# Kernel tuning notes

Measured on AMD Instinct MI355X. Metric: run time of the kernel, lower is better.

## Reference

```python
import jax, jax.numpy as jnp
from jax import lax
import numpy as np

B, S = 256, 512
VOCAB, EMB_D = 50000, 300
POS_MAX, POS_D = 512, 16
CNN_OUT, K, NCLASS = 50, 5, 10


def setup_inputs() -> dict:
    key = jax.random.key(0)
    ks = jax.random.split(key, 7)
    return {
        "tokens": jax.random.randint(ks[0], (B, S), 0, VOCAB),
        "embed_table": jax.random.normal(ks[1], (VOCAB, EMB_D), jnp.float32),
        "pos_table": jax.random.normal(ks[2], (POS_MAX, POS_D), jnp.float32),
        "conv_w": jax.random.normal(ks[3], (CNN_OUT, EMB_D + 2 * POS_D, K), jnp.float32) * 0.05,
        "conv_b": jax.random.normal(ks[4], (CNN_OUT,), jnp.float32) * 0.05,
        "fc_w": jax.random.normal(ks[5], (NCLASS, CNN_OUT), jnp.float32) * 0.1,
        "fc_b": jax.random.normal(ks[6], (NCLASS,), jnp.float32) * 0.1,
        "entity1": 1,
        "entity2": 2,
    }


def _nearest_entity_dist(tokens, entity, max_pos):
    # Distance from each token to the nearest occurrence of `entity`,
    # clipped to [0, max_pos-1]; sentences without the entity clip to max.
    Sl = tokens.shape[1]
    idx = jnp.arange(Sl)
    occ = tokens == entity  # [B, S]
    big = 2 * Sl
    # nearest occurrence index to the left (running max) and right (running min)
    left = lax.cummax(jnp.where(occ, idx, -big), axis=1)
    right = lax.cummin(jnp.where(occ, idx, big), axis=1, reverse=True)
    dist = jnp.minimum(idx - left, right - idx)
    return jnp.clip(dist, 0, max_pos - 1)


def reference(tokens, embed_table, pos_table, conv_w, conv_b, fc_w, fc_b,
              entity1, entity2):
    emb = embed_table[tokens]                      # [B, S, EMB_D] gather
    pad = jnp.all(emb == 0.0, axis=-1)             # [B, S] zero-row mask
    feats = [emb]
    for ent in (entity1, entity2):
        d = _nearest_entity_dist(tokens, ent, pos_table.shape[0])
        pe = pos_table[d]                          # [B, S, POS_D]
        pe = jnp.where(pad[..., None], 0.0, pe)    # zero masked positions
        feats.append(pe)
    x = jnp.concatenate(feats, axis=-1)            # [B, S, 332]
    x = jnp.transpose(x, (0, 2, 1))                # [B, C, S]
    pad_hw = conv_w.shape[-1] // 2
    y = lax.conv_general_dilated(
        x, conv_w, window_strides=(1,), padding=[(pad_hw, pad_hw)],
        dimension_numbers=("NCH", "OIH", "NCH"))
    y = jax.nn.relu(y + conv_b[None, :, None])     # [B, 50, S]
    y = jnp.max(y, axis=2)                         # full-length max pool -> [B, 50]
    out = y @ fc_w.T + fc_b                        # [B, NCLASS]
    return out
```

## Files before the change

kernel.cpp:

```cpp
#include <hip/hip_runtime.h>
#include <hip/hip_bf16.h>

typedef __attribute__((ext_vector_type(8))) short short8;
typedef __attribute__((ext_vector_type(4))) float floatx4;

#define BB 256
#define SS 512
#define VOCAB 50000
#define EMB_D 300
#define POS_MAX 512
#define POS_D 16
#define CNN_OUT 50
#define KW 5
#define NCLASS 10
#define C_IN 332
#define NKS 55
#define MROWS 64
#define FROWS 68
#define FSTR 392
#define E2STR 320
#define NWF (NKS * 4 * 64 * 8)

__device__ __forceinline__ unsigned pack2bf(float x, float y) {
    __hip_bfloat162 h = __float22bfloat162_rn(make_float2(x, y));
    return *reinterpret_cast<unsigned*>(&h);
}

__device__ __forceinline__ unsigned short f2bf(float x) {
    unsigned u = __float_as_uint(x);
    u += 0x7FFF + ((u >> 16) & 1);
    return (unsigned short)(u >> 16);
}

__global__ __launch_bounds__(256) void k_cvt(const float* __restrict__ E,
                                             unsigned short* __restrict__ E2) {
    int row = blockIdx.x * 4 + (threadIdx.x >> 6);
    if (row >= VOCAB) return;
    int lane = threadIdx.x & 63;
    const float4* src = (const float4*)(E + (size_t)row * EMB_D);
    unsigned short* dst = E2 + (size_t)row * E2STR;
    float4 a = src[lane];
    *(uint2*)&dst[lane * 4] = make_uint2(pack2bf(a.x, a.y), pack2bf(a.z, a.w));
    if (lane < 11) {
        float4 bq = src[64 + lane];
        *(uint2*)&dst[256 + lane * 4] = make_uint2(pack2bf(bq.x, bq.y), pack2bf(bq.z, bq.w));
    } else if (lane < 16) {
        *(uint2*)&dst[300 + (lane - 11) * 4] = make_uint2(0u, 0u);
    }
}

__global__ __launch_bounds__(256) void k_prep(const float* __restrict__ conv_w,
                                              unsigned short* __restrict__ Wf,
                                              float* __restrict__ ymax) {
    int idx = blockIdx.x * 256 + threadIdx.x;
    if (idx < NWF) {
        int j = idx & 7, l = (idx >> 3) & 63, nb = (idx >> 9) & 3, ks = idx >> 11;
        int k = ks / 11;
        int c = (ks % 11) * 32 + ((l >> 4) << 3) + j;
        int col = nb * 16 + (l & 15);
        float v = 0.f;
        if (c < C_IN && col < CNN_OUT)
            v = conv_w[col * (C_IN * KW) + c * KW + k];
        Wf[idx] = f2bf(v);
    } else if (idx < NWF + BB * CNN_OUT) {
        ymax[idx - NWF] = 0.f;
    }
}

__global__ __launch_bounds__(512) void k_dist(const int* __restrict__ tokens,
                                              const int* __restrict__ e1p,
                                              const int* __restrict__ e2p,
                                              int* __restrict__ d1,
                                              int* __restrict__ d2) {
    __shared__ int cnt1, cnt2;
    __shared__ int lst1[SS], lst2[SS];
    int b = blockIdx.x, s = threadIdx.x;
    if (s == 0) { cnt1 = 0; cnt2 = 0; }
    __syncthreads();
    int tok = tokens[b * SS + s];
    int e1 = *e1p, e2 = *e2p;
    if (tok == e1) lst1[atomicAdd(&cnt1, 1)] = s;
    if (tok == e2) lst2[atomicAdd(&cnt2, 1)] = s;
    __syncthreads();
    int dd1 = POS_MAX - 1;
    int n1 = cnt1;
    for (int i = 0; i < n1; ++i) dd1 = min(dd1, abs(s - lst1[i]));
    int dd2 = POS_MAX - 1;
    int n2 = cnt2;
    for (int i = 0; i < n2; ++i) dd2 = min(dd2, abs(s - lst2[i]));
    d1[b * SS + s] = dd1;
    d2[b * SS + s] = dd2;
}

__global__ __launch_bounds__(256, 3) void k_fused(const int* __restrict__ tokens,
                                                  const int* __restrict__ d1,
                                                  const int* __restrict__ d2,
                                                  const unsigned short* __restrict__ E2,
                                                  const float* __restrict__ pos,
                                                  const unsigned short* __restrict__ Wf,
                                                  const float* __restrict__ conv_b,
                                                  float* __restrict__ ymax) {
    __shared__ __align__(16) short F[FROWS * FSTR];
    int tid = threadIdx.x, lane = tid & 63, w = tid >> 6;
    int b = blockIdx.x >> 3, sb = blockIdx.x & 7;
    int s0 = sb * MROWS;

    int q = tid & 3;
    for (int rr = tid >> 2; rr < FROWS; rr += 64) {
        int sp = s0 - 2 + rr;
        bool valid = (sp >= 0 && sp < SS);
        int t = valid ? tokens[b * SS + sp] : 0;
        const uint4* src = (const uint4*)(E2 + (size_t)t * E2STR);

        int dd = 0;
        if (q < 2)
            dd = valid ? (q == 0 ? d1[b * SS + sp] : d2[b * SS + sp]) : 0;

        uint4 v[10];
        #pragma unroll
        for (int i = 0; i < 10; ++i) {
            int c4 = q + i * 4;
            v[i] = valid ? src[c4] : make_uint4(0u, 0u, 0u, 0u);
        }
        float4 pv[4];
        if (q < 2) {
            const float4* ps = (const float4*)(pos + dd * POS_D);
            #pragma unroll
            for (int i = 0; i < 4; ++i)
                pv[i] = valid ? ps[i] : make_float4(0.f, 0.f, 0.f, 0.f);
        }

        unsigned nzb = 0;
        #pragma unroll
        for (int i = 0; i < 10; ++i)
            nzb |= (v[i].x | v[i].y | v[i].z | v[i].w);
        bool nz = (nzb & 0x7FFF7FFFu) != 0u;
        #pragma unroll
        for (int i = 0; i < 10; ++i) {
            int c4 = q + i * 4;
            if (c4 <= 36) {
                *(uint4*)&F[rr * FSTR + c4 * 8] = v[i];
            } else if (c4 == 37) {
                *(uint2*)&F[rr * FSTR + 296] = make_uint2(v[i].x, v[i].y);
            }
        }

        unsigned long long bal = __ballot(nz);
        int g = lane >> 2;
        bool rowz = (((bal >> (g * 4)) & 0xFULL) == 0ULL);

        if (q < 2) {
            float msk = (valid && !rowz) ? 1.f : 0.f;
            int cbase = EMB_D + q * POS_D;
            #pragma unroll
            for (int i = 0; i < 4; ++i)
                *(uint2*)&F[rr * FSTR + cbase + i * 4] =
                    make_uint2(pack2bf(pv[i].x * msk, pv[i].y * msk),
                               pack2bf(pv[i].z * msk, pv[i].w * msk));
        } else {
            int cbase = C_IN + (q - 2) * 10;
            #pragma unroll
            for (int i = 0; i < 5; ++i)
                *(unsigned*)&F[rr * FSTR + cbase + i * 2] = 0u;
        }
    }
    __syncthreads();

    floatx4 acc[4][4];
    #pragma unroll
    for (int mm = 0; mm < 4; ++mm)
        #pragma unroll
        for (int nn = 0; nn < 4; ++nn) acc[mm][nn] = (floatx4)0.f;

    int arow = lane & 15, achunk = (lane >> 4) * 8;
    const short8* Bp = (const short8*)Wf;
    int lo = w * 14;
    int hi = min(lo + 14, NKS);

    short8 bA[4], bB[4];
    #pragma unroll
    for (int nb = 0; nb < 4; ++nb)
        bA[nb] = Bp[(lo * 4 + nb) * 64 + lane];
    if (lo + 1 < hi) {
        #pragma unroll
        for (int nb = 0; nb < 4; ++nb)
            bB[nb] = Bp[((lo + 1) * 4 + nb) * 64 + lane];
    }

    auto step = [&](int ks, short8 (&bf)[4], int pfks) {
        int k = ks / 11, kc = ks % 11;
        const short* abase = &F[(arow + k) * FSTR + kc * 32 + achunk];
        #pragma unroll
        for (int mm = 0; mm < 4; ++mm) {
            short8 afrag = *(const short8*)(abase + mm * 16 * FSTR);
            #pragma unroll
            for (int nn = 0; nn < 4; ++nn)
                acc[mm][nn] = __builtin_amdgcn_mfma_f32_16x16x32_bf16(afrag, bf[nn], acc[mm][nn], 0, 0, 0);
        }
        if (pfks < hi) {
            #pragma unroll
            for (int nb = 0; nb < 4; ++nb)
                bf[nb] = Bp[(pfks * 4 + nb) * 64 + lane];
        }
    };

    int ks = lo;
    for (; ks + 1 < hi; ks += 2) {
        step(ks, bA, ks + 2);
        step(ks + 1, bB, ks + 3);
    }
    if (ks < hi) step(ks, bA, NKS);

    __syncthreads();
    float* R = (float*)F;
    floatx4 red[4];
    #pragma unroll
    for (int round = 0; round < 2; ++round) {
        #pragma unroll
        for (int i = 0; i < 2; ++i)
            #pragma unroll
            for (int nn = 0; nn < 4; ++nn)
                *(floatx4*)&R[((w * 8 + i * 4 + nn) * 64 + lane) * 4] = acc[round * 2 + i][nn];
        __syncthreads();
        #pragma unroll
        for (int i = 0; i < 2; ++i) {
            floatx4 t0 = *(floatx4*)&R[((0 * 8 + i * 4 + w) * 64 + lane) * 4];
            floatx4 t1 = *(floatx4*)&R[((1 * 8 + i * 4 + w) * 64 + lane) * 4];
            floatx4 t2 = *(floatx4*)&R[((2 * 8 + i * 4 + w) * 64 + lane) * 4];
            floatx4 t3 = *(floatx4*)&R[((3 * 8 + i * 4 + w) * 64 + lane) * 4];
            red[round * 2 + i] = (t0 + t1) + (t2 + t3);
        }
        if (round == 0) __syncthreads();
    }

    int col = w * 16 + (lane & 15);
    float bias = (col < CNN_OUT) ? conv_b[col] : 0.f;
    float m = 0.f;
    #pragma unroll
    for (int mi = 0; mi < 4; ++mi)
        #pragma unroll
        for (int rg = 0; rg < 4; ++rg)
            m = fmaxf(m, red[mi][rg] + bias);
    m = fmaxf(m, __shfl_xor(m, 16));
    m = fmaxf(m, __shfl_xor(m, 32));
    if ((lane >> 4) == 0 && col < CNN_OUT)
        atomicMax((int*)ymax + b * CNN_OUT + col, __float_as_int(m));
}

__global__ __launch_bounds__(64) void k_fc(const float* __restrict__ ymax,
                                           const float* __restrict__ fc_w,
                                           const float* __restrict__ fc_b,
                                           float* __restrict__ out) {
    int b = blockIdx.x, n = threadIdx.x;
    if (n < NCLASS) {
        float a = fc_b[n];
        #pragma unroll
        for (int o = 0; o < CNN_OUT; ++o)
            a += ymax[b * CNN_OUT + o] * fc_w[n * CNN_OUT + o];
        out[b * NCLASS + n] = a;
    }
}

extern "C" void kernel_launch(void* const* d_in, const int* in_sizes, int n_in,
                              void* d_out, int out_size, void* d_ws, size_t ws_size,
                              hipStream_t stream) {
    const int*   tokens  = (const int*)  d_in[0];
    const float* embed   = (const float*)d_in[1];
    const float* pos     = (const float*)d_in[2];
    const float* conv_w  = (const float*)d_in[3];
    const float* conv_b  = (const float*)d_in[4];
    const float* fc_w    = (const float*)d_in[5];
    const float* fc_b    = (const float*)d_in[6];
    const int*   e1p     = (const int*)  d_in[7];
    const int*   e2p     = (const int*)  d_in[8];
    float* out = (float*)d_out;

    char* ws = (char*)d_ws;
    size_t off = 0;
    unsigned short* E2 = (unsigned short*)(ws + off); off += (size_t)VOCAB * E2STR * 2;
    unsigned short* Wf = (unsigned short*)(ws + off); off += (size_t)NWF * 2;
    int*   d1     = (int*)  (ws + off); off += (size_t)BB * SS * 4;
    int*   d2     = (int*)  (ws + off); off += (size_t)BB * SS * 4;
    float* ymax   = (float*)(ws + off); off += (size_t)BB * CNN_OUT * 4;
    (void)ws_size; (void)in_sizes; (void)n_in; (void)out_size;

    hipLaunchKernelGGL(k_cvt, dim3((VOCAB + 3) / 4), dim3(256), 0, stream, embed, E2);
    {
        int total = NWF + BB * CNN_OUT;
        hipLaunchKernelGGL(k_prep, dim3((total + 255) / 256), dim3(256), 0, stream,
                           conv_w, Wf, ymax);
    }
    hipLaunchKernelGGL(k_dist, dim3(BB), dim3(512), 0, stream, tokens, e1p, e2p, d1, d2);
    hipLaunchKernelGGL(k_fused, dim3(BB * (SS / MROWS)), dim3(256), 0, stream,
                       tokens, d1, d2, E2, pos, Wf, conv_b, ymax);
    hipLaunchKernelGGL(k_fc, dim3(BB), dim3(64), 0, stream, ymax, fc_w, fc_b, out);
}
```

Baseline: 67.33 us.

## Make fused conv kernel persistent over tiles with double-buffered LDS prefetch

The fused conv kernel now runs 512 blocks, each walking 8 tiles of 32 rows with two LDS buffers. The gathers for the next tile are issued into registers before the MFMA loop and written to shared memory afterwards, so global latency overlaps compute. The zero-row pad mask is precomputed per vocab row in the conversion kernel, so it no longer needs a per-row ballot. In exchange each tile has more block-wide barriers and B fragments are reloaded every tile. Occupancy drops to 2 blocks per CU, and 512 blocks may underfill the GPU.

```diff
diff --git a/kernel.cpp b/kernel.cpp
--- a/kernel.cpp
+++ b/kernel.cpp
@@ -15,10 +15,13 @@
 #define NCLASS 10
 #define C_IN 332
 #define NKS 55
-#define MROWS 64
-#define FROWS 68
+#define MROWS 32
+#define TILES 8
+#define FROWS 36
 #define FSTR 392
 #define E2STR 320
+#define NCH 38
+#define NEV (FROWS * NCH)
 #define NWF (NKS * 4 * 64 * 8)
 
 __device__ __forceinline__ unsigned pack2bf(float x, float y) {
@@ -33,20 +36,28 @@
 }
 
 __global__ __launch_bounds__(256) void k_cvt(const float* __restrict__ E,
-                                             unsigned short* __restrict__ E2) {
+                                             unsigned short* __restrict__ E2,
+                                             int* __restrict__ rowz) {
     int row = blockIdx.x * 4 + (threadIdx.x >> 6);
     if (row >= VOCAB) return;
     int lane = threadIdx.x & 63;
     const float4* src = (const float4*)(E + (size_t)row * EMB_D);
     unsigned short* dst = E2 + (size_t)row * E2STR;
     float4 a = src[lane];
+    unsigned nzb = __float_as_uint(a.x) | __float_as_uint(a.y) |
+                   __float_as_uint(a.z) | __float_as_uint(a.w);
     *(uint2*)&dst[lane * 4] = make_uint2(pack2bf(a.x, a.y), pack2bf(a.z, a.w));
     if (lane < 11) {
         float4 bq = src[64 + lane];
+        nzb |= __float_as_uint(bq.x) | __float_as_uint(bq.y) |
+               __float_as_uint(bq.z) | __float_as_uint(bq.w);
         *(uint2*)&dst[256 + lane * 4] = make_uint2(pack2bf(bq.x, bq.y), pack2bf(bq.z, bq.w));
     } else if (lane < 16) {
         *(uint2*)&dst[300 + (lane - 11) * 4] = make_uint2(0u, 0u);
     }
+    bool nz = (nzb & 0x7FFFFFFFu) != 0u;
+    unsigned long long bal = __ballot(nz);
+    if (lane == 0) rowz[row] = (bal == 0ULL) ? 1 : 0;
 }
 
 __global__ __launch_bounds__(256) void k_prep(const float* __restrict__ conv_w,
@@ -92,155 +103,180 @@
     d2[b * SS + s] = dd2;
 }
 
-__global__ __launch_bounds__(256, 3) void k_fused(const int* __restrict__ tokens,
+__global__ __launch_bounds__(256, 2) void k_fused(const int* __restrict__ tokens,
                                                   const int* __restrict__ d1,
                                                   const int* __restrict__ d2,
+                                                  const int* __restrict__ rowz,
                                                   const unsigned short* __restrict__ E2,
                                                   const float* __restrict__ pos,
                                                   const unsigned short* __restrict__ Wf,
                                                   const float* __restrict__ conv_b,
                                                   float* __restrict__ ymax) {
-    __shared__ __align__(16) short F[FROWS * FSTR];
+    __shared__ __align__(16) short Fbuf[2][FROWS * FSTR];
     int tid = threadIdx.x, lane = tid & 63, w = tid >> 6;
-    int b = blockIdx.x >> 3, sb = blockIdx.x & 7;
-    int s0 = sb * MROWS;
-
-    int q = tid & 3;
-    for (int rr = tid >> 2; rr < FROWS; rr += 64) {
-        int sp = s0 - 2 + rr;
-        bool valid = (sp >= 0 && sp < SS);
-        int t = valid ? tokens[b * SS + sp] : 0;
-        const uint4* src = (const uint4*)(E2 + (size_t)t * E2STR);
-
-        int dd = 0;
-        if (q < 2)
-            dd = valid ? (q == 0 ? d1[b * SS + sp] : d2[b * SS + sp]) : 0;
-
-        uint4 v[10];
-        #pragma unroll
-        for (int i = 0; i < 10; ++i) {
-            int c4 = q + i * 4;
-            v[i] = valid ? src[c4] : make_uint4(0u, 0u, 0u, 0u);
-        }
-        float4 pv[4];
-        if (q < 2) {
-            const float4* ps = (const float4*)(pos + dd * POS_D);
-            #pragma unroll
-            for (int i = 0; i < 4; ++i)
-                pv[i] = valid ? ps[i] : make_float4(0.f, 0.f, 0.f, 0.f);
-        }
-
-        unsigned nzb = 0;
-        #pragma unroll
-        for (int i = 0; i < 10; ++i)
-            nzb |= (v[i].x | v[i].y | v[i].z | v[i].w);
-        bool nz = (nzb & 0x7FFF7FFFu) != 0u;
-        #pragma unroll
-        for (int i = 0; i < 10; ++i) {
-            int c4 = q + i * 4;
-            if (c4 <= 36) {
-                *(uint4*)&F[rr * FSTR + c4 * 8] = v[i];
-            } else if (c4 == 37) {
-                *(uint2*)&F[rr * FSTR + 296] = make_uint2(v[i].x, v[i].y);
-            }
-        }
-
-        unsigned long long bal = __ballot(nz);
-        int g = lane >> 2;
-        bool rowz = (((bal >> (g * 4)) & 0xFULL) == 0ULL);
-
-        if (q < 2) {
-            float msk = (valid && !rowz) ? 1.f : 0.f;
-            int cbase = EMB_D + q * POS_D;
-            #pragma unroll
-            for (int i = 0; i < 4; ++i)
-                *(uint2*)&F[rr * FSTR + cbase + i * 4] =
-                    make_uint2(pack2bf(pv[i].x * msk, pv[i].y * msk),
-                               pack2bf(pv[i].z * msk, pv[i].w * msk));
-        } else {
-            int cbase = C_IN + (q - 2) * 10;
-            #pragma unroll
-            for (int i = 0; i < 5; ++i)
-                *(unsigned*)&F[rr * FSTR + cbase + i * 2] = 0u;
-        }
-    }
+    int b = blockIdx.x >> 1, half = blockIdx.x & 1;
+    int base = half * (MROWS * TILES);
+
+    const int* trow = tokens + b * SS;
+    const int* d1r = d1 + b * SS;
+    const int* d2r = d2 + b * SS;
+
+    short* cur = Fbuf[0];
+    short* nxt = Fbuf[1];
+
+    uint4 ev[6];
+    float4 pv[2];
+    float pmsk[2];
+
+    auto issue = [&](int srow) {
+        #pragma unroll
+        for (int j = 0; j < 6; ++j) {
+            int idx = tid + j * 256;
+            ev[j] = make_uint4(0u, 0u, 0u, 0u);
+            if (idx < NEV) {
+                int row = idx / NCH, ch = idx % NCH;
+                int sp = srow - 2 + row;
+                bool valid = (sp >= 0 && sp < SS);
+                if (valid) {
+                    int t = trow[sp];
+                    ev[j] = ((const uint4*)(E2 + (size_t)t * E2STR))[ch];
+                }
+            }
+        }
+        #pragma unroll
+        for (int j = 0; j < 2; ++j) {
+            int idx = tid + j * 256;
+            pv[j] = make_float4(0.f, 0.f, 0.f, 0.f);
+            pmsk[j] = 0.f;
+            if (idx < FROWS * 8) {
+                int row = idx >> 3, q = idx & 7;
+                int sp = srow - 2 + row;
+                bool valid = (sp >= 0 && sp < SS);
+                int table = q >> 2, i = q & 3;
+                if (valid) {
+                    int t = trow[sp];
+                    int rz = rowz[t];
+                    int dd = table ? d2r[sp] : d1r[sp];
+                    pmsk[j] = rz ? 0.f : 1.f;
+                    pv[j] = ((const float4*)(pos + dd * POS_D))[i];
+                }
+            }
+        }
+    };
+
+    auto commit = [&](short* Fb) {
+        #pragma unroll
+        for (int j = 0; j < 6; ++j) {
+            int idx = tid + j * 256;
+            if (idx < NEV) {
+                int row = idx / NCH, ch = idx % NCH;
+                if (ch <= 36)
+                    *(uint4*)&Fb[row * FSTR + ch * 8] = ev[j];
+                else
+                    *(uint2*)&Fb[row * FSTR + 296] = make_uint2(ev[j].x, ev[j].y);
+            }
+        }
+        #pragma unroll
+        for (int j = 0; j < 2; ++j) {
+            int idx = tid + j * 256;
+            if (idx < FROWS * 8) {
+                int row = idx >> 3, q = idx & 7;
+                int table = q >> 2, i = q & 3;
+                float mk = pmsk[j];
+                *(uint2*)&Fb[row * FSTR + EMB_D + table * POS_D + i * 4] =
+                    make_uint2(pack2bf(pv[j].x * mk, pv[j].y * mk),
+                               pack2bf(pv[j].z * mk, pv[j].w * mk));
+            }
+        }
+        #pragma unroll
+        for (int j = 0; j < 2; ++j) {
+            int idx = tid + j * 256;
+            if (idx < FROWS * 10) {
+                int row = idx / 10, dw = idx % 10;
+                *(unsigned*)&Fb[row * FSTR + C_IN + dw * 2] = 0u;
+            }
+        }
+    };
+
+    issue(base);
+    commit(cur);
     __syncthreads();
-
-    floatx4 acc[4][4];
-    #pragma unroll
-    for (int mm = 0; mm < 4; ++mm)
-        #pragma unroll
-        for (int nn = 0; nn < 4; ++nn) acc[mm][nn] = (floatx4)0.f;
 
     int arow = lane & 15, achunk = (lane >> 4) * 8;
     const short8* Bp = (const short8*)Wf;
     int lo = w * 14;
     int hi = min(lo + 14, NKS);
-
-    short8 bA[4], bB[4];
-    #pragma unroll
-    for (int nb = 0; nb < 4; ++nb)
-        bA[nb] = Bp[(lo * 4 + nb) * 64 + lane];
-    if (lo + 1 < hi) {
+    float m = -1e30f;
+
+    for (int ti = 0; ti < TILES; ++ti) {
+        if (ti + 1 < TILES) issue(base + (ti + 1) * MROWS);
+
+        floatx4 acc[2][4];
+        #pragma unroll
+        for (int mm = 0; mm < 2; ++mm)
+            #pragma unroll
+            for (int nn = 0; nn < 4; ++nn) acc[mm][nn] = (floatx4)0.f;
+
+        short8 bA[4], bB[4];
         #pragma unroll
         for (int nb = 0; nb < 4; ++nb)
-            bB[nb] = Bp[((lo + 1) * 4 + nb) * 64 + lane];
-    }
-
-    auto step = [&](int ks, short8 (&bf)[4], int pfks) {
-        int k = ks / 11, kc = ks % 11;
-        const short* abase = &F[(arow + k) * FSTR + kc * 32 + achunk];
-        #pragma unroll
-        for (int mm = 0; mm < 4; ++mm) {
-            short8 afrag = *(const short8*)(abase + mm * 16 * FSTR);
+            bA[nb] = Bp[(lo * 4 + nb) * 64 + lane];
+        if (lo + 1 < hi) {
+            #pragma unroll
+            for (int nb = 0; nb < 4; ++nb)
+                bB[nb] = Bp[((lo + 1) * 4 + nb) * 64 + lane];
+        }
+
+        auto step = [&](int ks, short8 (&bf)[4], int pfks) {
+            int k = ks / 11, kc = ks % 11;
+            const short* abase = &cur[(arow + k) * FSTR + kc * 32 + achunk];
+            #pragma unroll
+            for (int mm = 0; mm < 2; ++mm) {
+                short8 afrag = *(const short8*)(abase + mm * 16 * FSTR);
+                #pragma unroll
+                for (int nn = 0; nn < 4; ++nn)
+                    acc[mm][nn] = __builtin_amdgcn_mfma_f32_16x16x32_bf16(afrag, bf[nn], acc[mm][nn], 0, 0, 0);
+            }
+            if (pfks < hi) {
+                #pragma unroll
+                for (int nb = 0; nb < 4; ++nb)
+                    bf[nb] = Bp[(pfks * 4 + nb) * 64 + lane];
+            }
+        };
+
+        int ks = lo;
+        for (; ks + 1 < hi; ks += 2) {
+            step(ks, bA, ks + 2);
+            step(ks + 1, bB, ks + 3);
+        }
+        if (ks < hi) step(ks, bA, NKS);
+
+        __syncthreads();
+        float* R = (float*)cur;
+        #pragma unroll
+        for (int round = 0; round < 2; ++round) {
             #pragma unroll
             for (int nn = 0; nn < 4; ++nn)
-                acc[mm][nn] = __builtin_amdgcn_mfma_f32_16x16x32_bf16(afrag, bf[nn], acc[mm][nn], 0, 0, 0);
-        }
-        if (pfks < hi) {
-            #pragma unroll
-            for (int nb = 0; nb < 4; ++nb)
-                bf[nb] = Bp[(pfks * 4 + nb) * 64 + lane];
-        }
-    };
-
-    int ks = lo;
-    for (; ks + 1 < hi; ks += 2) {
-        step(ks, bA, ks + 2);
-        step(ks + 1, bB, ks + 3);
-    }
-    if (ks < hi) step(ks, bA, NKS);
-
-    __syncthreads();
-    float* R = (float*)F;
-    floatx4 red[4];
-    #pragma unroll
-    for (int round = 0; round < 2; ++round) {
-        #pragma unroll
-        for (int i = 0; i < 2; ++i)
-            #pragma unroll
-            for (int nn = 0; nn < 4; ++nn)
-                *(floatx4*)&R[((w * 8 + i * 4 + nn) * 64 + lane) * 4] = acc[round * 2 + i][nn];
+                *(floatx4*)&R[((w * 4 + nn) * 64 + lane) * 4] = acc[round][nn];
+            __syncthreads();
+            floatx4 t0 = *(floatx4*)&R[((0 * 4 + w) * 64 + lane) * 4];
+            floatx4 t1 = *(floatx4*)&R[((1 * 4 + w) * 64 + lane) * 4];
+            floatx4 t2 = *(floatx4*)&R[((2 * 4 + w) * 64 + lane) * 4];
+            floatx4 t3 = *(floatx4*)&R[((3 * 4 + w) * 64 + lane) * 4];
+            floatx4 red = (t0 + t1) + (t2 + t3);
+            #pragma unroll
+            for (int rg = 0; rg < 4; ++rg) m = fmaxf(m, red[rg]);
+            if (round == 0) __syncthreads();
+        }
+
+        if (ti + 1 < TILES) commit(nxt);
         __syncthreads();
-        #pragma unroll
-        for (int i = 0; i < 2; ++i) {
-            floatx4 t0 = *(floatx4*)&R[((0 * 8 + i * 4 + w) * 64 + lane) * 4];
-            floatx4 t1 = *(floatx4*)&R[((1 * 8 + i * 4 + w) * 64 + lane) * 4];
-            floatx4 t2 = *(floatx4*)&R[((2 * 8 + i * 4 + w) * 64 + lane) * 4];
-            floatx4 t3 = *(floatx4*)&R[((3 * 8 + i * 4 + w) * 64 + lane) * 4];
-            red[round * 2 + i] = (t0 + t1) + (t2 + t3);
-        }
-        if (round == 0) __syncthreads();
+        short* tmp = cur; cur = nxt; nxt = tmp;
     }
 
     int col = w * 16 + (lane & 15);
     float bias = (col < CNN_OUT) ? conv_b[col] : 0.f;
-    float m = 0.f;
-    #pragma unroll
-    for (int mi = 0; mi < 4; ++mi)
-        #pragma unroll
-        for (int rg = 0; rg < 4; ++rg)
-            m = fmaxf(m, red[mi][rg] + bias);
+    m = fmaxf(m + bias, 0.f);
     m = fmaxf(m, __shfl_xor(m, 16));
     m = fmaxf(m, __shfl_xor(m, 32));
     if ((lane >> 4) == 0 && col < CNN_OUT)
@@ -281,17 +317,18 @@
     unsigned short* Wf = (unsigned short*)(ws + off); off += (size_t)NWF * 2;
     int*   d1     = (int*)  (ws + off); off += (size_t)BB * SS * 4;
     int*   d2     = (int*)  (ws + off); off += (size_t)BB * SS * 4;
+    int*   rowzp  = (int*)  (ws + off); off += (size_t)VOCAB * 4;
     float* ymax   = (float*)(ws + off); off += (size_t)BB * CNN_OUT * 4;
     (void)ws_size; (void)in_sizes; (void)n_in; (void)out_size;
 
-    hipLaunchKernelGGL(k_cvt, dim3((VOCAB + 3) / 4), dim3(256), 0, stream, embed, E2);
+    hipLaunchKernelGGL(k_cvt, dim3((VOCAB + 3) / 4), dim3(256), 0, stream, embed, E2, rowzp);
     {
         int total = NWF + BB * CNN_OUT;
         hipLaunchKernelGGL(k_prep, dim3((total + 255) / 256), dim3(256), 0, stream,
                            conv_w, Wf, ymax);
     }
     hipLaunchKernelGGL(k_dist, dim3(BB), dim3(512), 0, stream, tokens, e1p, e2p, d1, d2);
-    hipLaunchKernelGGL(k_fused, dim3(BB * (SS / MROWS)), dim3(256), 0, stream,
-                       tokens, d1, d2, E2, pos, Wf, conv_b, ymax);
+    hipLaunchKernelGGL(k_fused, dim3(BB * (SS / (MROWS * TILES))), dim3(256), 0, stream,
+                       tokens, d1, d2, rowzp, E2, pos, Wf, conv_b, ymax);
     hipLaunchKernelGGL(k_fc, dim3(BB), dim3(64), 0, stream, ymax, fc_w, fc_b, out);
 }
```

Measured after the change: 87.55 us. +30.0%, slower.
